# Kernel tuning notes

Measured on AMD Instinct MI355X. Metric: run time of the kernel, lower is better.

## Reference

```python
import jax, jax.numpy as jnp
import numpy as np

N = 100000      # nodes
E = 500000      # edges
F_IN = 165      # Elliptic feature dim
HID = 128       # hidden
HEADS = 2
DH = HID // HEADS  # 64, per-head GAT out dim
EPS = 1e-5


def setup_inputs() -> dict:
    key = jax.random.key(0)
    ks = jax.random.split(key, 40)

    def w(k, shape, fan_in):
        return (jax.random.normal(k, shape, jnp.float32) / np.sqrt(fan_in)).astype(jnp.float32)

    def bn_params(k, d):
        k1, k2 = jax.random.split(k)
        return (jnp.ones((d,), jnp.float32),                       # gamma
                jnp.zeros((d,), jnp.float32),                      # beta
                0.1 * jax.random.normal(k1, (d,), jnp.float32),    # running mean
                jax.random.uniform(k2, (d,), jnp.float32, 0.5, 1.5))  # running var

    bn1 = bn_params(ks[10], HID)
    bn2 = bn_params(ks[11], HID)
    bn3 = bn_params(ks[12], DH)

    return {
        "x": jax.random.normal(ks[0], (N, F_IN), jnp.float32),
        "edge_index": jax.random.randint(ks[1], (2, E), 0, N, jnp.int32),
        # input_proj
        "w_in": w(ks[2], (F_IN, HID), F_IN), "b_in": jnp.zeros((HID,), jnp.float32),
        # GCNConv
        "w_gcn": w(ks[3], (HID, HID), HID), "b_gcn": jnp.zeros((HID,), jnp.float32),
        "bn1_g": bn1[0], "bn1_b": bn1[1], "bn1_m": bn1[2], "bn1_v": bn1[3],
        # GATConv (heads=2, out=64, concat)
        "w_gat": w(ks[4], (HID, HEADS * DH), HID),
        "att_src": 0.1 * jax.random.normal(ks[5], (HEADS, DH), jnp.float32),
        "att_dst": 0.1 * jax.random.normal(ks[6], (HEADS, DH), jnp.float32),
        "b_gat": jnp.zeros((HEADS * DH,), jnp.float32),
        "bn2_g": bn2[0], "bn2_b": bn2[1], "bn2_m": bn2[2], "bn2_v": bn2[3],
        # SAGEConv (mean aggr)
        "w_sage_l": w(ks[7], (HID, DH), HID), "b_sage": jnp.zeros((DH,), jnp.float32),
        "w_sage_r": w(ks[8], (HID, DH), HID),
        "bn3_g": bn3[0], "bn3_b": bn3[1], "bn3_m": bn3[2], "bn3_v": bn3[3],
        # residual proj + classifier
        "w_res": w(ks[9], (HID, DH), HID), "b_res": jnp.zeros((DH,), jnp.float32),
        "w_c1": w(ks[13], (DH, 32), DH), "b_c1": jnp.zeros((32,), jnp.float32),
        "w_c2": w(ks[14], (32, 2), 32), "b_c2": jnp.zeros((2,), jnp.float32),
    }


def _bn(h, g, b, m, v):
    # eval-mode BatchNorm1d with running stats
    return (h - m) * (g / jnp.sqrt(v + EPS)) + b


def reference(x, edge_index, w_in, b_in, w_gcn, b_gcn,
              bn1_g, bn1_b, bn1_m, bn1_v,
              w_gat, att_src, att_dst, b_gat,
              bn2_g, bn2_b, bn2_m, bn2_v,
              w_sage_l, b_sage, w_sage_r,
              bn3_g, bn3_b, bn3_m, bn3_v,
              w_res, b_res, w_c1, b_c1, w_c2, b_c2):
    n = x.shape[0]
    src, dst = edge_index[0], edge_index[1]
    loop = jnp.arange(n, dtype=src.dtype)
    src_l = jnp.concatenate([src, loop])   # edges + self loops (GCN & GAT)
    dst_l = jnp.concatenate([dst, loop])

    # ---- input_proj (dropout = identity in eval) ----
    h = jax.nn.elu(x @ w_in + b_in)
    residual = h

    hw = h @ w_gcn
    deg = jax.ops.segment_sum(jnp.ones_like(dst_l, jnp.float32), dst_l, n)
    dinv = jnp.where(deg > 0, jax.lax.rsqrt(deg), 0.0)
    norm = dinv[src_l] * dinv[dst_l]                      # [E+N]
    h1 = jax.ops.segment_sum(hw[src_l] * norm[:, None], dst_l, n) + b_gcn
    h1 = jax.nn.elu(_bn(h1, bn1_g, bn1_b, bn1_m, bn1_v))

    # ---- GATConv (heads=2, concat, self loops, leaky_relu 0.2) ----
    g = (h1 @ w_gat).reshape(n, HEADS, DH)
    a_src = jnp.sum(g * att_src, axis=-1)                 # [N, H]
    a_dst = jnp.sum(g * att_dst, axis=-1)
    e = jax.nn.leaky_relu(a_src[src_l] + a_dst[dst_l], 0.2)   # [E+N, H]
    mx = jax.ops.segment_max(e, dst_l, n)                 # per-dst softmax max
    ex = jnp.exp(e - mx[dst_l])
    denom = jax.ops.segment_sum(ex, dst_l, n)
    alpha = ex / (denom[dst_l] + 1e-16)                   # [E+N, H]
    h2 = jax.ops.segment_sum(g[src_l] * alpha[:, :, None], dst_l, n)
    h2 = h2.reshape(n, HEADS * DH) + b_gat
    h2 = jax.nn.elu(_bn(h2, bn2_g, bn2_b, bn2_m, bn2_v))

    # ---- SAGEConv: W_l mean(neighbors) + W_r x + b (no self loops) ----
    deg_s = jax.ops.segment_sum(jnp.ones_like(dst, jnp.float32), dst, n)
    mean_nb = jax.ops.segment_sum(h2[src], dst, n) / jnp.maximum(deg_s, 1.0)[:, None]
    h3 = mean_nb @ w_sage_l + b_sage + h2 @ w_sage_r
    h3 = _bn(h3, bn3_g, bn3_b, bn3_m, bn3_v)
    h3 = jax.nn.elu(h3 + residual @ w_res + b_res)

    # ---- classifier ----
    z = jax.nn.elu(h3 @ w_c1 + b_c1)
    return z @ w_c2 + b_c2
```

## Files before the change

kernel.cpp:

```cpp
#include <hip/hip_runtime.h>
#include <cstdint>
#include <cstddef>

#define BN_EPS 1e-5f

typedef __attribute__((ext_vector_type(8))) short short8v;
typedef __attribute__((ext_vector_type(4))) float float4v;
typedef __attribute__((ext_vector_type(4))) unsigned int uint4v;
typedef unsigned int uint32;
typedef unsigned short ushort16;

__device__ __forceinline__ float elu_f(float v){ return v > 0.f ? v : expm1f(v); }
__device__ __forceinline__ float leaky_f(float v){ return v > 0.f ? v : 0.2f*v; }
__device__ __forceinline__ uint32 f2bf(float f){
  uint32 b = __float_as_uint(f);
  return (b + 0x7fffu + ((b >> 16) & 1u)) >> 16;
}
__device__ __forceinline__ float bflo(uint32 u){ return __uint_as_float(u << 16); }
__device__ __forceinline__ float bfhi(uint32 u){ return __uint_as_float(u & 0xffff0000u); }
__device__ __forceinline__ float readlane_f(float v, int l){
  return __int_as_float(__builtin_amdgcn_readlane(__float_as_int(v), l));
}


__global__ void count_deg_kernel(const int* __restrict__ dst, int E, int* __restrict__ cnt){
  int i = blockIdx.x*blockDim.x + threadIdx.x;
  if(i < E) atomicAdd(&cnt[dst[i]], 1);
}

__global__ __launch_bounds__(1024) void scan_blocks(const int* __restrict__ cnt, int n,
                                                    int* __restrict__ part, int* __restrict__ bsum){
  __shared__ int wsum[16];
  int tid = threadIdx.x, lane = tid & 63, w = tid >> 6;
  int i = blockIdx.x*1024 + tid;
  int v = (i < n) ? cnt[i] : 0;
  int sv = v;
#pragma unroll
  for(int o = 1; o < 64; o <<= 1){
    int u = __shfl_up(sv, o);
    if(lane >= o) sv += u;
  }
  if(lane == 63) wsum[w] = sv;
  __syncthreads();
  int woff = 0;
#pragma unroll
  for(int q = 0; q < 16; q++) woff += (q < w) ? wsum[q] : 0;
  if(i < n) part[i] = woff + sv - v;
  if(tid == 1023) bsum[blockIdx.x] = woff + sv;
}

__global__ __launch_bounds__(1024) void scan_bsum(const int* __restrict__ bsum, int nb,
                                                  int* __restrict__ boff, int* __restrict__ rowptr, int n){
  __shared__ int wsum[16];
  int tid = threadIdx.x, lane = tid & 63, w = tid >> 6;
  int v = (tid < nb) ? bsum[tid] : 0;
  int sv = v;
#pragma unroll
  for(int o = 1; o < 64; o <<= 1){
    int u = __shfl_up(sv, o);
    if(lane >= o) sv += u;
  }
  if(lane == 63) wsum[w] = sv;
  __syncthreads();
  int woff = 0;
#pragma unroll
  for(int q = 0; q < 16; q++) woff += (q < w) ? wsum[q] : 0;
  if(tid < nb) boff[tid] = woff + sv - v;
  if(tid == 1023) rowptr[n] = woff + sv;
}

__global__ void scan_add_dinv(const int* __restrict__ part, const int* __restrict__ boff,
                              const int* __restrict__ cnt, int n,
                              int* __restrict__ rowptr, float* __restrict__ dinv){
  int i = blockIdx.x*blockDim.x + threadIdx.x;
  if(i < n){
    rowptr[i] = part[i] + boff[i >> 10];
    dinv[i] = rsqrtf((float)cnt[i] + 1.0f);
  }
}

__global__ void scatter_kernel(const int* __restrict__ src, const int* __restrict__ dst, int E,
                               const int* __restrict__ rowptr, int* __restrict__ fill,
                               int* __restrict__ col){
  int i = blockIdx.x*blockDim.x + threadIdx.x;
  if(i < E){
    int s = src[i], d = dst[i];
    int p = rowptr[d] + atomicAdd(&fill[d], 1);
    col[p] = s;
  }
}


__global__ __launch_bounds__(256) void cvt_x(const float* __restrict__ x, uint2* __restrict__ xb, int total){
  int idx = blockIdx.x*256 + threadIdx.x;
  if(idx >= total) return;
  int row = idx/48;
  int cp = idx - row*48;
  int c = cp*4;
  const float* xr = x + (size_t)row*165;
  float v0 = (c   < 165) ? xr[c]   : 0.f;
  float v1 = (c+1 < 165) ? xr[c+1] : 0.f;
  float v2 = (c+2 < 165) ? xr[c+2] : 0.f;
  float v3 = (c+3 < 165) ? xr[c+3] : 0.f;
  xb[idx] = make_uint2(f2bf(v0) | (f2bf(v1) << 16), f2bf(v2) | (f2bf(v3) << 16));
}


__global__ void prep_scales(const float* __restrict__ bn1_g, const float* __restrict__ bn1_b,
    const float* __restrict__ bn1_m, const float* __restrict__ bn1_v, const float* __restrict__ b_gcn,
    const float* __restrict__ bn2_g, const float* __restrict__ bn2_b,
    const float* __restrict__ bn2_m, const float* __restrict__ bn2_v, const float* __restrict__ b_gat,
    const float* __restrict__ att_s, const float* __restrict__ att_d,
    const float* __restrict__ bn3_g, const float* __restrict__ bn3_b,
    const float* __restrict__ bn3_m, const float* __restrict__ bn3_v,
    const float* __restrict__ b_sage, const float* __restrict__ b_res,
    float* __restrict__ s1, float* __restrict__ b1c,
    float* __restrict__ s2, float* __restrict__ b2c,
    float* __restrict__ atts2, float* __restrict__ attd2,
    float* __restrict__ s3, float* __restrict__ bias3){
  int c = threadIdx.x;
  float v1 = bn1_g[c]*rsqrtf(bn1_v[c] + BN_EPS);
  s1[c] = v1;
  b1c[c] = (b_gcn[c] - bn1_m[c])*v1 + bn1_b[c];
  float v2 = bn2_g[c]*rsqrtf(bn2_v[c] + BN_EPS);
  s2[c] = v2;
  b2c[c] = (b_gat[c] - bn2_m[c])*v2 + bn2_b[c];
  atts2[c] = att_s[c]/v2;
  attd2[c] = att_d[c]/v2;
  if(c < 64){
    float v3 = bn3_g[c]*rsqrtf(bn3_v[c] + BN_EPS);
    s3[c] = v3;
    bias3[c] = (b_sage[c] - bn3_m[c])*v3 + bn3_b[c] + b_res[c];
  }
}


__device__ __forceinline__ void pack_region(const float* __restrict__ W, int K, int NOUT, int kbase, int idx,
                                            const float* __restrict__ scale, ushort16* __restrict__ out){
  int k = idx / NOUT, c = idx - k*NOUT;
  float v = (k < K) ? W[(size_t)k*NOUT + c] : 0.f;
  if(scale) v *= scale[c];
  int pk = kbase + k;
  out[(size_t)(pk >> 3)*NOUT*8 + (size_t)c*8 + (pk & 7)] = (ushort16)f2bf(v);
}

__global__ __launch_bounds__(256) void pack_all(const float* __restrict__ w_in, const float* __restrict__ w_gcn,
    const float* __restrict__ w_gat, const float* __restrict__ w_sl, const float* __restrict__ w_sr,
    const float* __restrict__ w_res,
    const float* __restrict__ s1, const float* __restrict__ s2, const float* __restrict__ s3,
    ushort16* __restrict__ pw_in, ushort16* __restrict__ pw_gcn,
    ushort16* __restrict__ pw_gat, ushort16* __restrict__ pw_cat){
  int b = blockIdx.x, t = threadIdx.x;
  if(b < 96)       pack_region(w_in,  165, 128, 0,   b*256 + t,        nullptr, pw_in);
  else if(b < 160) pack_region(w_gcn, 128, 128, 0,   (b-96)*256 + t,   s1,      pw_gcn);
  else if(b < 224) pack_region(w_gat, 128, 128, 0,   (b-160)*256 + t,  s2,      pw_gat);
  else if(b < 256) pack_region(w_sl,  128, 64,  0,   (b-224)*256 + t,  s3,      pw_cat);
  else if(b < 288) pack_region(w_sr,  128, 64,  128, (b-256)*256 + t,  s3,      pw_cat);
  else             pack_region(w_res, 128, 64,  256, (b-288)*256 + t,  nullptr, pw_cat);
}


template<int KSTEPS, int NOUT, int EPI>
__global__ __launch_bounds__(256) void mfma_gemm(
    const ushort16* __restrict__ A, int lda,
    const uint4v* __restrict__ pw,
    const float* __restrict__ bias,
    void* __restrict__ out, int ldo, int N,
    const float* __restrict__ dinv,
    const float* __restrict__ atts2, const float* __restrict__ attd2,
    float* __restrict__ a_src, float* __restrict__ a_dst,
    float* __restrict__ ess)
{
  constexpr int LDSV = KSTEPS*4*NOUT;
  __shared__ uint4v wlds[LDSV];
  int t = threadIdx.x;
#pragma unroll
  for(int q = 0; q < LDSV/256; q++)
    wlds[q*256 + t] = pw[q*256 + t];
  __syncthreads();

  int wid = t >> 6, lane = t & 63;
  int wm, wn;
  if(NOUT == 128){ wm = wid >> 1; wn = wid & 1; } else { wm = wid; wn = 0; }
  constexpr int MTILE = (NOUT == 128) ? 128 : 256;
  long row0 = (long)blockIdx.x*MTILE + wm*64;
  int l15 = lane & 15, lk = lane >> 4;
  int wn64 = wn*64;
  const ushort16* wl = (const ushort16*)wlds;

  float4v acc[4][4];
#pragma unroll
  for(int fm = 0; fm < 4; fm++)
#pragma unroll
    for(int fn = 0; fn < 4; fn++) acc[fm][fn] = (float4v){0.f,0.f,0.f,0.f};

  const ushort16* abase[4];
#pragma unroll
  for(int fm = 0; fm < 4; fm++){
    long r = row0 + fm*16 + l15;
    if(r > (long)N - 1) r = (long)N - 1;
    abase[fm] = A + r*(size_t)lda + lk*8;
  }

  short8v a[4];
#pragma unroll
  for(int fm = 0; fm < 4; fm++) a[fm] = *(const short8v*)(abase[fm]);

#pragma unroll
  for(int ks = 0; ks < KSTEPS; ks++){
    short8v b[4];
#pragma unroll
    for(int fn = 0; fn < 4; fn++){
      int c = wn64 + fn*16 + l15;
      b[fn] = *(const short8v*)(wl + ((size_t)((ks*4 + lk)*NOUT + c))*8);
    }
    short8v an[4];
    if(ks + 1 < KSTEPS){
#pragma unroll
      for(int fm = 0; fm < 4; fm++) an[fm] = *(const short8v*)(abase[fm] + (ks + 1)*32);
    }
#pragma unroll
    for(int fm = 0; fm < 4; fm++)
#pragma unroll
      for(int fn = 0; fn < 4; fn++)
        acc[fm][fn] = __builtin_amdgcn_mfma_f32_16x16x32_bf16(a[fm], b[fn], acc[fm][fn], 0, 0, 0);
    if(ks + 1 < KSTEPS){
#pragma unroll
      for(int fm = 0; fm < 4; fm++) a[fm] = an[fm];
    }
  }

#pragma unroll
  for(int fm = 0; fm < 4; fm++){
#pragma unroll
    for(int rr = 0; rr < 4; rr++){
      long r = row0 + fm*16 + lk*4 + rr;
      if(r < N){
        float dr = 0.f;
        if constexpr(EPI == 4) dr = dinv[r];
#pragma unroll
        for(int fn = 0; fn < 4; fn++){
          int c = wn64 + fn*16 + l15;
          float v = acc[fm][fn][rr];
          if constexpr(EPI == 1){ v += bias[c]; v = elu_f(v); }
          if constexpr(EPI == 4){ v *= dr; }
          ((ushort16*)out)[r*(size_t)ldo + c] = (ushort16)f2bf(v);
        }
      }
    }
  }

  if constexpr(EPI == 3){
    float as2[4], ad2[4];
#pragma unroll
    for(int fn = 0; fn < 4; fn++){
      int c = wn64 + fn*16 + l15;
      as2[fn] = atts2[c]; ad2[fn] = attd2[c];
    }
#pragma unroll
    for(int fm = 0; fm < 4; fm++){
#pragma unroll
      for(int rr = 0; rr < 4; rr++){
        float p1 = 0.f, p2 = 0.f;
#pragma unroll
        for(int fn = 0; fn < 4; fn++){
          p1 += acc[fm][fn][rr]*as2[fn];
          p2 += acc[fm][fn][rr]*ad2[fn];
        }
#pragma unroll
        for(int o = 1; o < 16; o <<= 1){
          p1 += __shfl_xor(p1, o);
          p2 += __shfl_xor(p2, o);
        }
        long r = row0 + fm*16 + lk*4 + rr;
        if(l15 == 0 && r < N){
          a_src[2*r + wn] = p1;
          a_dst[2*r + wn] = p2;
          ess[2*r + wn] = __expf(leaky_f(p1 + p2));
        }
      }
    }
  }
}


__global__ __launch_bounds__(256) void gcn_agg(const uint32* __restrict__ hw2,
    const int* __restrict__ rowptr, const int* __restrict__ col,
    const float* __restrict__ dinv, const float* __restrict__ b1c,
    uint32* __restrict__ h1, int N)
{
  int t = threadIdx.x & 63;
  int w = __builtin_amdgcn_readfirstlane(threadIdx.x >> 6);
  float2 bc = ((const float2*)b1c)[t];
  int stride = gridDim.x*8;
  for(int i0 = (blockIdx.x*4 + w)*2; i0 < N; i0 += stride){
    int i1 = i0 + 1;
    bool has1 = i1 < N;
    int beg0 = rowptr[i0];
    int end0 = rowptr[i0+1];
    int beg1 = end0;
    int end1 = has1 ? rowptr[i1+1] : end0;
    float di0 = dinv[i0];
    float di1 = has1 ? dinv[i1] : 0.f;
    uint32 su0 = hw2[(size_t)i0*64 + t];
    float a00 = bflo(su0), a01 = bfhi(su0);
    float a10 = 0.f, a11 = 0.f;
    if(has1){ uint32 su1 = hw2[(size_t)i1*64 + t]; a10 = bflo(su1); a11 = bfhi(su1); }
#define R0(q) { int row = __builtin_amdgcn_readlane(s0, q); \
    uint32 u = hw2[(size_t)row*64 + t]; a00 += bflo(u); a01 += bfhi(u); }
#define R1(q) { int row = __builtin_amdgcn_readlane(s1, q); \
    uint32 u = hw2[(size_t)row*64 + t]; a10 += bflo(u); a11 += bfhi(u); }
    for(int c0 = beg0, c1 = beg1; c0 < end0 || c1 < end1; c0 += 64, c1 += 64){
      int p0 = c0 + t, p1 = c1 + t;
      int s0 = (p0 < end0) ? col[p0] : 0;
      int s1 = (p1 < end1) ? col[p1] : 0;
      int cl0 = end0 - c0; cl0 = cl0 < 0 ? 0 : (cl0 > 64 ? 64 : cl0);
      int cl1 = end1 - c1; cl1 = cl1 < 0 ? 0 : (cl1 > 64 ? 64 : cl1);
      int m = cl0 < cl1 ? cl0 : cl1;
      int q = 0;
      for(; q + 2 <= m; q += 2){ R0(q) R1(q) R0(q+1) R1(q+1) }
      for(; q < m; q++){ R0(q) R1(q) }
      for(int qa = m; qa < cl0; qa++){ R0(qa) }
      for(int qb = m; qb < cl1; qb++){ R1(qb) }
    }
#undef R0
#undef R1
    h1[(size_t)i0*64 + t] = f2bf(elu_f(a00*di0 + bc.x)) | (f2bf(elu_f(a01*di0 + bc.y)) << 16);
    if(has1)
      h1[(size_t)i1*64 + t] = f2bf(elu_f(a10*di1 + bc.x)) | (f2bf(elu_f(a11*di1 + bc.y)) << 16);
  }
}


__global__ __launch_bounds__(256) void gat_gather(const uint32* __restrict__ g,
    const int* __restrict__ rowptr, const int* __restrict__ col,
    const float* __restrict__ a_src, const float* __restrict__ a_dst,
    const float* __restrict__ ess, const float* __restrict__ b2c,
    uint32* __restrict__ h2out, int N)
{
  int t = threadIdx.x & 63;
  int w = __builtin_amdgcn_readfirstlane(threadIdx.x >> 6);
  float2 bc = ((const float2*)b2c)[t];
  int hl = t >> 5;
  int stride = gridDim.x*4;
  for(int i = blockIdx.x*4 + w; i < N; i += stride){
    int beg = rowptr[i], end = rowptr[i+1];
    int deg = end - beg;
    float2 ad = ((const float2*)a_dst)[i];
    float sw0 = ess[2*i], sw1 = ess[2*i+1];
    float d0 = 0.f, d1 = 0.f, a0 = 0.f, a1 = 0.f;
#define GAT_ROWF(q) { int row = __builtin_amdgcn_readlane(s, q); \
    float w0q = readlane_f(e0, q); \
    float w1q = readlane_f(e1, q); \
    float wq = hl ? w1q : w0q; \
    uint32 u = g[(size_t)row*64 + t]; a0 += wq*bflo(u); a1 += wq*bfhi(u); }
    if(deg <= 64){
      int p = beg + t;
      int s = 0; float e0 = 0.f, e1 = 0.f;
      if(p < end){
        s = col[p];
        float2 as = ((const float2*)a_src)[s];
        e0 = __expf(leaky_f(as.x + ad.x));
        e1 = __expf(leaky_f(as.y + ad.y));
      }
      d0 = e0; d1 = e1;
      int q = 0;
      for(; q + 4 <= deg; q += 4){ GAT_ROWF(q) GAT_ROWF(q+1) GAT_ROWF(q+2) GAT_ROWF(q+3) }
      for(; q < deg; q++){ GAT_ROWF(q) }
    } else {
      for(int c0 = beg; c0 < end; c0 += 64){
        int p = c0 + t;
        int cl = end - c0; if(cl > 64) cl = 64;
        float e0 = 0.f, e1 = 0.f; int s = 0;
        if(p < end){
          s = col[p];
          float2 as = ((const float2*)a_src)[s];
          e0 = __expf(leaky_f(as.x + ad.x));
          e1 = __expf(leaky_f(as.y + ad.y));
        }
        d0 += e0; d1 += e1;
        int q = 0;
        for(; q + 4 <= cl; q += 4){ GAT_ROWF(q) GAT_ROWF(q+1) GAT_ROWF(q+2) GAT_ROWF(q+3) }
        for(; q < cl; q++){ GAT_ROWF(q) }
      }
    }
#undef GAT_ROWF
#pragma unroll
    for(int o = 32; o > 0; o >>= 1){ d0 += __shfl_xor(d0, o); d1 += __shfl_xor(d1, o); }
    float rD = 1.f/(((hl ? d1 : d0) + (hl ? sw1 : sw0)) + 1e-16f);
    float sw = hl ? sw1 : sw0;
    uint32 su = g[(size_t)i*64 + t];
    float v0 = (a0 + sw*bflo(su))*rD + bc.x;
    float v1 = (a1 + sw*bfhi(su))*rD + bc.y;
    h2out[(size_t)i*192 + t] = f2bf(elu_f(v0)) | (f2bf(elu_f(v1)) << 16);
  }
}


__global__ __launch_bounds__(256) void sage_mean(const uint32* __restrict__ h2,
    const int* __restrict__ rowptr, const int* __restrict__ col,
    uint32* __restrict__ mout, int N)
{
  int t = threadIdx.x & 63;
  int w = __builtin_amdgcn_readfirstlane(threadIdx.x >> 6);
  int stride = gridDim.x*8;
  for(int i0 = (blockIdx.x*4 + w)*2; i0 < N; i0 += stride){
    int i1 = i0 + 1;
    bool has1 = i1 < N;
    int beg0 = rowptr[i0];
    int end0 = rowptr[i0+1];
    int beg1 = end0;
    int end1 = has1 ? rowptr[i1+1] : end0;
    float a00 = 0.f, a01 = 0.f, a10 = 0.f, a11 = 0.f;
#define S0(q) { int row = __builtin_amdgcn_readlane(s0, q); \
    uint32 u = h2[(size_t)row*192 + t]; a00 += bflo(u); a01 += bfhi(u); }
#define S1(q) { int row = __builtin_amdgcn_readlane(s1, q); \
    uint32 u = h2[(size_t)row*192 + t]; a10 += bflo(u); a11 += bfhi(u); }
    for(int c0 = beg0, c1 = beg1; c0 < end0 || c1 < end1; c0 += 64, c1 += 64){
      int p0 = c0 + t, p1 = c1 + t;
      int s0 = (p0 < end0) ? col[p0] : 0;
      int s1 = (p1 < end1) ? col[p1] : 0;
      int cl0 = end0 - c0; cl0 = cl0 < 0 ? 0 : (cl0 > 64 ? 64 : cl0);
      int cl1 = end1 - c1; cl1 = cl1 < 0 ? 0 : (cl1 > 64 ? 64 : cl1);
      int m = cl0 < cl1 ? cl0 : cl1;
      int q = 0;
      for(; q + 2 <= m; q += 2){ S0(q) S1(q) S0(q+1) S1(q+1) }
      for(; q < m; q++){ S0(q) S1(q) }
      for(int qa = m; qa < cl0; qa++){ S0(qa) }
      for(int qb = m; qb < cl1; qb++){ S1(qb) }
    }
#undef S0
#undef S1
    float inv0 = 1.f/fmaxf((float)(end0 - beg0), 1.f);
    mout[(size_t)i0*192 + t] = f2bf(a00*inv0) | (f2bf(a01*inv0) << 16);
    if(has1){
      float inv1 = 1.f/fmaxf((float)(end1 - beg1), 1.f);
      mout[(size_t)i1*192 + t] = f2bf(a10*inv1) | (f2bf(a11*inv1) << 16);
    }
  }
}


__global__ __launch_bounds__(256) void classifier_kernel(const uint32* __restrict__ h3,
    const float* __restrict__ w1, const float* __restrict__ b1,
    const float* __restrict__ w2, const float* __restrict__ b2,
    float* __restrict__ out, int N)
{
  __shared__ float hs[8][64];
  __shared__ float zs[8][32];
  int node0 = blockIdx.x*8;
  int t = threadIdx.x;
  {
    int r = t >> 5, cp = t & 31;
    int nd = node0 + r;
    uint32 u = (nd < N) ? h3[(size_t)nd*32 + cp] : 0u;
    hs[r][2*cp]   = bflo(u);
    hs[r][2*cp+1] = bfhi(u);
  }
  __syncthreads();
  int nn = t >> 5, ln = t & 31;
  float acc = b1[ln];
#pragma unroll
  for(int k = 0; k < 64; k++) acc += hs[nn][k]*w1[k*32 + ln];
  zs[nn][ln] = elu_f(acc);
  __syncthreads();
  int node = node0 + nn;
  if(ln < 2 && node < N){
    float o = b2[ln];
#pragma unroll
    for(int k = 0; k < 32; k++) o += zs[nn][k]*w2[k*2 + ln];
    out[(size_t)node*2 + ln] = o;
  }
}


extern "C" void kernel_launch(void* const* d_in, const int* in_sizes, int n_in,
                              void* d_out, int out_size, void* d_ws, size_t ws_size,
                              hipStream_t stream)
{
  (void)n_in; (void)out_size; (void)ws_size;
  const float* x      = (const float*)d_in[0];
  const int*   ei     = (const int*)  d_in[1];
  const float* w_in   = (const float*)d_in[2];
  const float* b_in   = (const float*)d_in[3];
  const float* w_gcn  = (const float*)d_in[4];
  const float* b_gcn  = (const float*)d_in[5];
  const float* bn1_g  = (const float*)d_in[6];
  const float* bn1_b  = (const float*)d_in[7];
  const float* bn1_m  = (const float*)d_in[8];
  const float* bn1_v  = (const float*)d_in[9];
  const float* w_gat  = (const float*)d_in[10];
  const float* att_s  = (const float*)d_in[11];
  const float* att_d  = (const float*)d_in[12];
  const float* b_gat  = (const float*)d_in[13];
  const float* bn2_g  = (const float*)d_in[14];
  const float* bn2_b  = (const float*)d_in[15];
  const float* bn2_m  = (const float*)d_in[16];
  const float* bn2_v  = (const float*)d_in[17];
  const float* w_sl   = (const float*)d_in[18];
  const float* b_sage = (const float*)d_in[19];
  const float* w_sr   = (const float*)d_in[20];
  const float* bn3_g  = (const float*)d_in[21];
  const float* bn3_b  = (const float*)d_in[22];
  const float* bn3_m  = (const float*)d_in[23];
  const float* bn3_v  = (const float*)d_in[24];
  const float* w_res  = (const float*)d_in[25];
  const float* b_res  = (const float*)d_in[26];
  const float* w_c1   = (const float*)d_in[27];
  const float* b_c1   = (const float*)d_in[28];
  const float* w_c2   = (const float*)d_in[29];
  const float* b_c2   = (const float*)d_in[30];

  const int F_IN = 165;
  int N = in_sizes[0]/F_IN;
  int E = in_sizes[1]/2;
  const int* srcp = ei;
  const int* dstp = ei + E;
  int nb = (N + 1023) >> 10;

  char* p = (char*)d_ws;
  auto alloc = [&](size_t bytes) -> char* {
    char* q = p; p += (bytes + 255) & ~(size_t)255; return q;
  };
  ushort16* Acat  = (ushort16*)alloc((size_t)N*384*2);
  ushort16* xb    = (ushort16*)alloc((size_t)N*192*2);
  ushort16* bufG  = (ushort16*)alloc((size_t)N*128*2);
  float* a_src    = (float*)alloc((size_t)N*2*4);
  float* a_dst    = (float*)alloc((size_t)N*2*4);
  float* ess      = (float*)alloc((size_t)N*2*4);
  float* dinv     = (float*)alloc((size_t)N*4);
  int* cnt        = (int*)alloc((size_t)N*4);
  int* fill       = (int*)alloc((size_t)N*4);
  int* rowptr     = (int*)alloc((size_t)(N+1)*4);
  int* part       = (int*)alloc((size_t)N*4);
  int* bsum       = (int*)alloc(1024*4);
  int* boff       = (int*)alloc(1024*4);
  int* col        = (int*)alloc((size_t)E*4);
  float* s1       = (float*)alloc(128*4);
  float* b1c      = (float*)alloc(128*4);
  float* s2       = (float*)alloc(128*4);
  float* b2c      = (float*)alloc(128*4);
  float* atts2    = (float*)alloc(128*4);
  float* attd2    = (float*)alloc(128*4);
  float* s3       = (float*)alloc(64*4);
  float* bias3    = (float*)alloc(64*4);
  ushort16* pw_in  = (ushort16*)alloc(6*4*128*16);
  ushort16* pw_gcn = (ushort16*)alloc(4*4*128*16);
  ushort16* pw_gat = (ushort16*)alloc(4*4*128*16);
  ushort16* pw_cat = (ushort16*)alloc(12*4*64*16);

  ushort16* h1 = xb;
  ushort16* h3 = bufG;

  hipMemsetAsync(cnt, 0, (size_t)((char*)(fill + N) - (char*)cnt), stream);

  count_deg_kernel<<<(E+255)/256, 256, 0, stream>>>(dstp, E, cnt);
  scan_blocks<<<nb, 1024, 0, stream>>>(cnt, N, part, bsum);
  scan_bsum<<<1, 1024, 0, stream>>>(bsum, nb, boff, rowptr, N);
  scan_add_dinv<<<(N+255)/256, 256, 0, stream>>>(part, boff, cnt, N, rowptr, dinv);
  scatter_kernel<<<(E+255)/256, 256, 0, stream>>>(srcp, dstp, E, rowptr, fill, col);

  cvt_x<<<(N*48 + 255)/256, 256, 0, stream>>>(x, (uint2*)xb, N*48);
  prep_scales<<<1, 128, 0, stream>>>(bn1_g, bn1_b, bn1_m, bn1_v, b_gcn,
                                     bn2_g, bn2_b, bn2_m, bn2_v, b_gat,
                                     att_s, att_d,
                                     bn3_g, bn3_b, bn3_m, bn3_v, b_sage, b_res,
                                     s1, b1c, s2, b2c, atts2, attd2, s3, bias3);
  pack_all<<<320, 256, 0, stream>>>(w_in, w_gcn, w_gat, w_sl, w_sr, w_res,
                                    s1, s2, s3, pw_in, pw_gcn, pw_gat, pw_cat);

  int g128 = (N + 127)/128;
  int g256 = (N + 255)/256;
  int gagg = (N + 3)/4; if(gagg > 4096) gagg = 4096;
  int gpair = (N + 7)/8; if(gpair > 4096) gpair = 4096;

  mfma_gemm<6,128,1><<<g128, 256, 0, stream>>>(xb, 192, (const uint4v*)pw_in, b_in,
      (void*)(Acat + 256), 384, N, nullptr, nullptr, nullptr, nullptr, nullptr, nullptr);
  mfma_gemm<4,128,4><<<g128, 256, 0, stream>>>(Acat + 256, 384, (const uint4v*)pw_gcn, nullptr,
      (void*)bufG, 128, N, dinv, nullptr, nullptr, nullptr, nullptr, nullptr);
  gcn_agg<<<gpair, 256, 0, stream>>>((const uint32*)bufG, rowptr, col, dinv, b1c,
                                     (uint32*)h1, N);
  mfma_gemm<4,128,3><<<g128, 256, 0, stream>>>(h1, 128, (const uint4v*)pw_gat, nullptr,
      (void*)bufG, 128, N, nullptr, atts2, attd2, a_src, a_dst, ess);
  gat_gather<<<gagg, 256, 0, stream>>>((const uint32*)bufG, rowptr, col, a_src, a_dst, ess,
                                       b2c, (uint32*)Acat + 64, N);
  sage_mean<<<gpair, 256, 0, stream>>>((const uint32*)Acat + 64, rowptr, col, (uint32*)Acat, N);
  mfma_gemm<12,64,1><<<g256, 256, 0, stream>>>(Acat, 384, (const uint4v*)pw_cat, bias3,
      (void*)h3, 64, N, nullptr, nullptr, nullptr, nullptr, nullptr, nullptr);
  classifier_kernel<<<(N+7)/8, 256, 0, stream>>>((const uint32*)h3, w_c1, b_c1, w_c2, b_c2,
                                                 (float*)d_out, N);
}
```

Before: 332.7 us.

## Double-buffer weight slices in LDS and transpose MFMA outputs for vector stores

The GEMM kernel no longer loads the whole packed weight matrix into LDS before starting. It now streams one K-slice at a time into a two-slot LDS buffer, with a register prefetch of the next slice overlapping the MFMAs. The MFMA operands are swapped so each lane holds four consecutive output columns of one row. That lets the epilogue write packed 4-element bf16 stores and cuts the attention-logit reduction to two shuffles. It adds a __syncthreads per K step and lowers LDS use, which may raise occupancy.

```diff
diff --git a/kernel.cpp b/kernel.cpp
--- a/kernel.cpp
+++ b/kernel.cpp
@@ -171,14 +171,10 @@
     float* __restrict__ a_src, float* __restrict__ a_dst,
     float* __restrict__ ess)
 {
-  constexpr int LDSV = KSTEPS*4*NOUT;
-  __shared__ uint4v wlds[LDSV];
+  constexpr int SLICE = 4*NOUT;
+  constexpr int PT = SLICE/256;
+  __shared__ uint4v wlds[2][SLICE];
   int t = threadIdx.x;
-#pragma unroll
-  for(int q = 0; q < LDSV/256; q++)
-    wlds[q*256 + t] = pw[q*256 + t];
-  __syncthreads();
-
   int wid = t >> 6, lane = t & 63;
   int wm, wn;
   if(NOUT == 128){ wm = wid >> 1; wn = wid & 1; } else { wm = wid; wn = 0; }
@@ -186,7 +182,6 @@
   long row0 = (long)blockIdx.x*MTILE + wm*64;
   int l15 = lane & 15, lk = lane >> 4;
   int wn64 = wn*64;
-  const ushort16* wl = (const ushort16*)wlds;
 
   float4v acc[4][4];
 #pragma unroll
@@ -202,18 +197,26 @@
     abase[fm] = A + r*(size_t)lda + lk*8;
   }
 
+  uint4v rst[PT];
+#pragma unroll
+  for(int i = 0; i < PT; i++) rst[i] = pw[i*256 + t];
+#pragma unroll
+  for(int i = 0; i < PT; i++) wlds[0][i*256 + t] = rst[i];
+  if(KSTEPS > 1){
+#pragma unroll
+    for(int i = 0; i < PT; i++) rst[i] = pw[SLICE + i*256 + t];
+  }
   short8v a[4];
 #pragma unroll
   for(int fm = 0; fm < 4; fm++) a[fm] = *(const short8v*)(abase[fm]);
+  __syncthreads();
 
 #pragma unroll
   for(int ks = 0; ks < KSTEPS; ks++){
     short8v b[4];
 #pragma unroll
-    for(int fn = 0; fn < 4; fn++){
-      int c = wn64 + fn*16 + l15;
-      b[fn] = *(const short8v*)(wl + ((size_t)((ks*4 + lk)*NOUT + c))*8);
-    }
+    for(int fn = 0; fn < 4; fn++)
+      b[fn] = *(const short8v*)&wlds[ks & 1][lk*NOUT + wn64 + fn*16 + l15];
     short8v an[4];
     if(ks + 1 < KSTEPS){
 #pragma unroll
@@ -223,61 +226,68 @@
     for(int fm = 0; fm < 4; fm++)
 #pragma unroll
       for(int fn = 0; fn < 4; fn++)
-        acc[fm][fn] = __builtin_amdgcn_mfma_f32_16x16x32_bf16(a[fm], b[fn], acc[fm][fn], 0, 0, 0);
+        acc[fm][fn] = __builtin_amdgcn_mfma_f32_16x16x32_bf16(b[fn], a[fm], acc[fm][fn], 0, 0, 0);
     if(ks + 1 < KSTEPS){
 #pragma unroll
+      for(int i = 0; i < PT; i++) wlds[(ks + 1) & 1][i*256 + t] = rst[i];
+      if(ks + 2 < KSTEPS){
+#pragma unroll
+        for(int i = 0; i < PT; i++) rst[i] = pw[(size_t)(ks + 2)*SLICE + i*256 + t];
+      }
+#pragma unroll
       for(int fm = 0; fm < 4; fm++) a[fm] = an[fm];
     }
+    __syncthreads();
   }
 
 #pragma unroll
   for(int fm = 0; fm < 4; fm++){
-#pragma unroll
-    for(int rr = 0; rr < 4; rr++){
-      long r = row0 + fm*16 + lk*4 + rr;
-      if(r < N){
-        float dr = 0.f;
-        if constexpr(EPI == 4) dr = dinv[r];
-#pragma unroll
-        for(int fn = 0; fn < 4; fn++){
-          int c = wn64 + fn*16 + l15;
-          float v = acc[fm][fn][rr];
-          if constexpr(EPI == 1){ v += bias[c]; v = elu_f(v); }
-          if constexpr(EPI == 4){ v *= dr; }
-          ((ushort16*)out)[r*(size_t)ldo + c] = (ushort16)f2bf(v);
+    long r = row0 + fm*16 + l15;
+    if(r < N){
+      float dr = 0.f;
+      if constexpr(EPI == 4) dr = dinv[r];
+#pragma unroll
+      for(int fn = 0; fn < 4; fn++){
+        int c0 = wn64 + fn*16 + lk*4;
+        float v0 = acc[fm][fn][0], v1 = acc[fm][fn][1];
+        float v2 = acc[fm][fn][2], v3 = acc[fm][fn][3];
+        if constexpr(EPI == 1){
+          float4 bs = *(const float4*)(bias + c0);
+          v0 = elu_f(v0 + bs.x); v1 = elu_f(v1 + bs.y);
+          v2 = elu_f(v2 + bs.z); v3 = elu_f(v3 + bs.w);
         }
+        if constexpr(EPI == 4){ v0 *= dr; v1 *= dr; v2 *= dr; v3 *= dr; }
+        uint2 ov = make_uint2(f2bf(v0) | (f2bf(v1) << 16), f2bf(v2) | (f2bf(v3) << 16));
+        *(uint2*)((ushort16*)out + r*(size_t)ldo + c0) = ov;
       }
     }
   }
 
   if constexpr(EPI == 3){
-    float as2[4], ad2[4];
+    float4 asv[4], adv[4];
 #pragma unroll
     for(int fn = 0; fn < 4; fn++){
-      int c = wn64 + fn*16 + l15;
-      as2[fn] = atts2[c]; ad2[fn] = attd2[c];
+      int c0 = wn64 + fn*16 + lk*4;
+      asv[fn] = *(const float4*)(atts2 + c0);
+      adv[fn] = *(const float4*)(attd2 + c0);
     }
 #pragma unroll
     for(int fm = 0; fm < 4; fm++){
-#pragma unroll
-      for(int rr = 0; rr < 4; rr++){
-        float p1 = 0.f, p2 = 0.f;
-#pragma unroll
-        for(int fn = 0; fn < 4; fn++){
-          p1 += acc[fm][fn][rr]*as2[fn];
-          p2 += acc[fm][fn][rr]*ad2[fn];
-        }
-#pragma unroll
-        for(int o = 1; o < 16; o <<= 1){
-          p1 += __shfl_xor(p1, o);
-          p2 += __shfl_xor(p2, o);
-        }
-        long r = row0 + fm*16 + lk*4 + rr;
-        if(l15 == 0 && r < N){
-          a_src[2*r + wn] = p1;
-          a_dst[2*r + wn] = p2;
-          ess[2*r + wn] = __expf(leaky_f(p1 + p2));
-        }
+      float p1 = 0.f, p2 = 0.f;
+#pragma unroll
+      for(int fn = 0; fn < 4; fn++){
+        p1 += acc[fm][fn][0]*asv[fn].x + acc[fm][fn][1]*asv[fn].y
+            + acc[fm][fn][2]*asv[fn].z + acc[fm][fn][3]*asv[fn].w;
+        p2 += acc[fm][fn][0]*adv[fn].x + acc[fm][fn][1]*adv[fn].y
+            + acc[fm][fn][2]*adv[fn].z + acc[fm][fn][3]*adv[fn].w;
+      }
+      p1 += __shfl_xor(p1, 16); p1 += __shfl_xor(p1, 32);
+      p2 += __shfl_xor(p2, 16); p2 += __shfl_xor(p2, 32);
+      long r = row0 + fm*16 + l15;
+      if(lane < 16 && r < N){
+        a_src[2*r + wn] = p1;
+        a_dst[2*r + wn] = p2;
+        ess[2*r + wn] = __expf(leaky_f(p1 + p2));
       }
     }
   }
```

Result: faster. 316.8 us (-4.8%).
